# Performance work log

Hardware: AMD Instinct MI355X
Metric: run time of the kernel (lower is better)

## Reference

```python
import jax, jax.numpy as jnp
import numpy as np

SCALE = 0.5          # centroids_input_scale
MAX_STRIDE = 16      # centroids_max_stride
CM_STRIDE = 2        # centroids_confmaps_stride (backbone overall stride)
THRESH = 0.2         # peak_threshold
CROP = 160           # crop_size
K = 32               # max peaks per sample (ragged -> dense+mask)
PATCH = 5            # integral-refinement patch size (sleap default)


def setup_inputs() -> dict:
    key = jax.random.key(0)
    k1, k2, k3 = jax.random.split(key, 3)
    full_imgs = jax.random.uniform(k1, (16, 1024, 1024, 1), jnp.float32)
    w1 = jax.random.normal(k2, (5, 5, 1, 32), jnp.float32) * 0.1
    b1 = jnp.zeros((32,), jnp.float32)
    w2 = jax.random.normal(k3, (5, 5, 32, 1), jnp.float32) * 0.1
    b2 = jnp.zeros((1,), jnp.float32)
    return {"full_imgs": full_imgs, "w1": w1, "b1": b1, "w2": w2, "b2": b2}


def _conv(x, w, stride):
    return jax.lax.conv_general_dilated(
        x, w, (stride, stride), 'SAME',
        dimension_numbers=('NHWC', 'HWIO', 'NHWC'))


def _centroid_model(x, w1, b1, w2, b2):
    h = jax.nn.relu(_conv(x, w1, CM_STRIDE) + b1)
    return jax.nn.sigmoid(_conv(h, w2, 1) + b2)  # [B,Hc,Wc,1]


def _forward(full_imgs, w1, b1, w2, b2):
    B, H, W, C = full_imgs.shape
    # --- resize_image + pad_to_stride ---
    hs, ws = int(H * SCALE), int(W * SCALE)
    imgs = jax.image.resize(full_imgs, (B, hs, ws, C), 'bilinear')
    ph, pw = (-hs) % MAX_STRIDE, (-ws) % MAX_STRIDE
    imgs = jnp.pad(imgs, ((0, 0), (0, ph), (0, pw), (0, 0)))
    # --- centroid confmaps ---
    cms = _centroid_model(imgs, w1, b1, w2, b2)[..., 0]  # [B,Hc,Wc]
    Hc, Wc = cms.shape[1], cms.shape[2]
    # --- find_local_peaks: 3x3 NMS + threshold, top-K per sample ---
    mx = jax.lax.reduce_window(cms, -jnp.inf, jax.lax.max,
                               (1, 3, 3), (1, 1, 1), 'SAME')
    is_peak = (cms >= mx) & (cms > THRESH)
    scores = jnp.where(is_peak, cms, -jnp.inf).reshape(B, -1)
    vals, idx = jax.lax.top_k(scores, K)            # [B,K]
    valid = jnp.isfinite(vals)                      # [B,K] bool
    py = idx // Wc
    px = idx % Wc
    # --- integral refinement over PATCH x PATCH (zero outside bounds) ---
    off = jnp.arange(PATCH) - (PATCH - 1) // 2      # [-2..2]
    yy = py[..., None, None] + off[None, None, :, None]   # [B,K,P,P]
    xx = px[..., None, None] + off[None, None, None, :]
    inb = (yy >= 0) & (yy < Hc) & (xx >= 0) & (xx < Wc)
    yc = jnp.clip(yy, 0, Hc - 1)
    xc = jnp.clip(xx, 0, Wc - 1)
    bidx = jnp.arange(B)[:, None, None, None]
    patches = cms[bidx, yc, xc] * inb               # [B,K,P,P]
    gv = patches.sum((-2, -1)) + 1e-12
    fo = off.astype(cms.dtype)
    dx = (patches * fo[None, None, None, :]).sum((-2, -1)) / gv
    dy = (patches * fo[None, None, :, None]).sum((-2, -1)) / gv
    # --- map back to full-image coords ---
    cx = (px.astype(cms.dtype) + dx) * CM_STRIDE / SCALE
    cy = (py.astype(cms.dtype) + dy) * CM_STRIDE / SCALE
    cx = jnp.where(valid, cx, CROP / 2)
    cy = jnp.where(valid, cy, CROP / 2)
    centroid_vals = jnp.where(valid, vals, 0.0)
    crop_offsets = jnp.stack([cx - CROP / 2, cy - CROP / 2], axis=-1)  # (x,y)
    # --- crop_bboxes: bilinear crop of CROPxCROP, (CROP-1)-pixel span ---
    gi = jnp.arange(CROP, dtype=cms.dtype)
    sy = (cy - (CROP - 1) / 2)[..., None] + gi      # [B,K,CROP] row coords
    sx = (cx - (CROP - 1) / 2)[..., None] + gi      # [B,K,CROP] col coords
    y0 = jnp.floor(sy); x0 = jnp.floor(sx)
    wy = (sy - y0)[..., :, None, None]              # [B,K,CROP,1,1]
    wx = (sx - x0)[..., None, :, None]              # [B,K,1,CROP,1]
    yi0 = jnp.clip(y0.astype(jnp.int32), 0, H - 1)
    yi1 = jnp.clip(y0.astype(jnp.int32) + 1, 0, H - 1)
    xi0 = jnp.clip(x0.astype(jnp.int32), 0, W - 1)
    xi1 = jnp.clip(x0.astype(jnp.int32) + 1, 0, W - 1)

    def gath(yi, xi):  # -> [B,K,CROP,CROP,C]
        return full_imgs[bidx, yi[..., :, None], xi[..., None, :], :]

    top = gath(yi0, xi0) * (1 - wx) + gath(yi0, xi1) * wx
    bot = gath(yi1, xi0) * (1 - wx) + gath(yi1, xi1) * wx
    crops = top * (1 - wy) + bot * wy
    # crop_and_resize extrapolation_value=0 outside the image
    inr = (((sy >= 0) & (sy <= H - 1))[..., :, None]
           & ((sx >= 0) & (sx <= W - 1))[..., None, :])
    crops = crops * inr[..., None] * valid[..., None, None, None]
    return crops, crop_offsets, centroid_vals, valid


def reference(full_imgs, w1, b1, w2, b2):
    return _forward(full_imgs, w1, b1, w2, b2)
```

## Files before the change

kernel.cpp:

```cpp
#include <hip/hip_runtime.h>
#include <math.h>

#define BATCH 16
#define HF 1024
#define WF 1024
#define HS 512
#define WS2 512
#define HC 256
#define WC 256
#define KMAX 32
#define CAP 16384
#define CROPSZ 160
#define CNT_STRIDE 16
#define NCHUNK 16
#define CHUNK 1024

#define OFF_IMGS 0UL
#define OFF_CMS  16777216UL
#define OFF_KEYS 20971520UL
#define OFF_CNT  23068672UL
#define OFF_CX   23070720UL
#define OFF_CY   (OFF_CX + 2048UL)
#define OFF_VLD  (OFF_CY + 2048UL)
#define OFF_CAND (OFF_VLD + 2048UL)

#define OUT_CROPS 0
#define OUT_OFFS  13107200
#define OUT_VALS  13108224
#define OUT_VALID 13108736

__global__ __launch_bounds__(256) void resize_kernel(const float* __restrict__ full,
                                                     float* __restrict__ imgs,
                                                     int* __restrict__ counts) {
    if (blockIdx.x == 0 && blockIdx.y == 0 && threadIdx.x < BATCH * CNT_STRIDE)
        counts[threadIdx.x] = 0;
    __shared__ float simg[10][1024];
    int tid = threadIdx.x;
    int y0 = blockIdx.x << 2;
    int b = blockIdx.y;
    const float* base = full + ((size_t)b << 20);
#pragma unroll
    for (int s = 0; s < 10; ++s) {
        int r = 2 * y0 - 1 + s;
        r = r < 0 ? 0 : (r > HF - 1 ? HF - 1 : r);
        ((float4*)simg[s])[tid] = ((const float4*)(base + r * WF))[tid];
    }
    __syncthreads();
    const float w4[4] = {0.125f, 0.375f, 0.375f, 0.125f};
#pragma unroll
    for (int p = 0; p < 2; ++p) {
        int x = tid + 256 * p;
        float wx[4];
        int rx[4];
        float sx = 0.f;
#pragma unroll
        for (int ii = 0; ii < 4; ++ii) {
            int c = 2 * x - 1 + ii;
            float wc = (c >= 0 && c < WF) ? w4[ii] : 0.f;
            wx[ii] = wc; sx += wc;
            rx[ii] = c < 0 ? 0 : (c >= WF ? WF - 1 : c);
        }
#pragma unroll
        for (int r = 0; r < 4; ++r) {
            int yy = y0 + r;
            float sy = 0.f;
            float wy[4];
#pragma unroll
            for (int j = 0; j < 4; ++j) {
                int rr = 2 * yy - 1 + j;
                float w = (rr >= 0 && rr < HF) ? w4[j] : 0.f;
                wy[j] = w; sy += w;
            }
            float acc = 0.f;
#pragma unroll
            for (int j = 0; j < 4; ++j) {
                float rowacc = 0.f;
                const float* sr = simg[2 * r + j];
#pragma unroll
                for (int ii = 0; ii < 4; ++ii) rowacc += wx[ii] * sr[rx[ii]];
                acc += wy[j] * rowacc;
            }
            imgs[((size_t)b << 18) + (yy << 9) + x] = acc * (1.f / (sy * sx));
        }
    }
}

__global__ __launch_bounds__(256) void conv_fused2_kernel(
    const float* __restrict__ imgs, const float* __restrict__ w1,
    const float* __restrict__ b1, const float* __restrict__ w2,
    const float* __restrict__ b2, float* __restrict__ cms) {
    __shared__ float simg[75][76];
    __shared__ float4 sh[36][37];
    int tid = threadIdx.x;
    int b = blockIdx.y;
    int Y0 = (blockIdx.x >> 3) << 5;
    int X0 = (blockIdx.x & 7) << 5;

    const float* ib = imgs + ((size_t)b << 18);
    int r0 = 2 * Y0 - 5, c0 = 2 * X0 - 5;
    for (int i = tid; i < 75 * 76; i += 256) {
        int r = i / 76, c = i - r * 76;
        int gy = r0 + r, gx = c0 + c;
        float v = 0.f;
        if ((unsigned)gy < 512u && (unsigned)gx < 512u)
            v = ib[(gy << 9) + gx];
        simg[r][c] = v;
    }

    bool c1act = tid < 216;
    int ghy = tid / 6;
    int ghx0 = (tid - ghy * 6) * 6;
    const float* c1base = &simg[2 * ghy][2 * ghx0];
    float4* shw = &sh[ghy][ghx0];
    bool rowok = (unsigned)(Y0 - 2 + ghy) < 256u;
    int gx0 = X0 - 2 + ghx0;

    int cx = tid & 31;
    int ry0 = (tid >> 5) << 2;
    const float4* hb = &sh[ry0][cx];
    float4 zv0 = make_float4(0.f, 0.f, 0.f, 0.f);
    float4 zv1 = zv0, zv2 = zv0, zv3 = zv0;

    for (int q = 0; q < 8; ++q) {
        float4 wq[25];
        const float4* w14 = (const float4*)w1;
#pragma unroll
        for (int t = 0; t < 25; ++t) wq[t] = w14[t * 8 + q];
        float4 bq = ((const float4*)b1)[q];

        __syncthreads();

        if (c1act) {
            float4 acc[6];
#pragma unroll
            for (int j = 0; j < 6; ++j) acc[j] = bq;
#pragma unroll
            for (int ky = 0; ky < 5; ++ky) {
                const float* rp = c1base + ky * 76;
                float4 f0 = *(const float4*)(rp);
                float4 f1 = *(const float4*)(rp + 4);
                float4 f2 = *(const float4*)(rp + 8);
                float4 f3 = *(const float4*)(rp + 12);
                float f[16] = {f0.x, f0.y, f0.z, f0.w, f1.x, f1.y, f1.z, f1.w,
                               f2.x, f2.y, f2.z, f2.w, f3.x, f3.y, f3.z, f3.w};
#pragma unroll
                for (int j = 0; j < 6; ++j)
#pragma unroll
                    for (int kx = 0; kx < 5; ++kx) {
                        float v = f[2 * j + kx];
                        float4 w = wq[ky * 5 + kx];
                        acc[j].x += v * w.x; acc[j].y += v * w.y;
                        acc[j].z += v * w.z; acc[j].w += v * w.w;
                    }
            }
#pragma unroll
            for (int j = 0; j < 6; ++j) {
                float4 r;
                bool ok = rowok && ((unsigned)(gx0 + j) < 256u);
                r.x = ok ? fmaxf(acc[j].x, 0.f) : 0.f;
                r.y = ok ? fmaxf(acc[j].y, 0.f) : 0.f;
                r.z = ok ? fmaxf(acc[j].z, 0.f) : 0.f;
                r.w = ok ? fmaxf(acc[j].w, 0.f) : 0.f;
                shw[j] = r;
            }
        }

        const float4* w24 = (const float4*)w2;
#pragma unroll
        for (int t = 0; t < 25; ++t) wq[t] = w24[t * 8 + q];

        __syncthreads();

#pragma unroll
        for (int rr = 0; rr < 8; ++rr) {
#pragma unroll
            for (int kx = 0; kx < 5; ++kx) {
                float4 hv = hb[rr * 37 + kx];
#pragma unroll
                for (int j = 0; j < 4; ++j) {
                    int ky = rr - j;
                    if (ky < 0 || ky > 4) continue;
                    float4 w = wq[ky * 5 + kx];
                    if (j == 0) {
                        zv0.x += hv.x * w.x; zv0.y += hv.y * w.y;
                        zv0.z += hv.z * w.z; zv0.w += hv.w * w.w;
                    } else if (j == 1) {
                        zv1.x += hv.x * w.x; zv1.y += hv.y * w.y;
                        zv1.z += hv.z * w.z; zv1.w += hv.w * w.w;
                    } else if (j == 2) {
                        zv2.x += hv.x * w.x; zv2.y += hv.y * w.y;
                        zv2.z += hv.z * w.z; zv2.w += hv.w * w.w;
                    } else {
                        zv3.x += hv.x * w.x; zv3.y += hv.y * w.y;
                        zv3.z += hv.z * w.z; zv3.w += hv.w * w.w;
                    }
                }
            }
        }
    }

    float bb = b2[0];
    float z0 = bb + zv0.x + zv0.y + zv0.z + zv0.w;
    float z1 = bb + zv1.x + zv1.y + zv1.z + zv1.w;
    float z2 = bb + zv2.x + zv2.y + zv2.z + zv2.w;
    float z3 = bb + zv3.x + zv3.y + zv3.z + zv3.w;
    size_t ob = ((size_t)b << 16) + ((size_t)(Y0 + ry0) << 8) + (X0 + cx);
    cms[ob]       = 1.f / (1.f + expf(-z0));
    cms[ob + 256] = 1.f / (1.f + expf(-z1));
    cms[ob + 512] = 1.f / (1.f + expf(-z2));
    cms[ob + 768] = 1.f / (1.f + expf(-z3));
}

__global__ __launch_bounds__(256) void peak_scan_kernel(
    const float* __restrict__ cms, unsigned long long* __restrict__ keys,
    int* __restrict__ counts) {
    int b = blockIdx.x >> 8;
    int y = blockIdx.x & 255;
    int x = threadIdx.x;
    const float* cb = cms + ((size_t)b << 16);
    __shared__ float rows[3][256];
    __shared__ int lcnt, lbase;
    if (x == 0) lcnt = 0;
#pragma unroll
    for (int j = 0; j < 3; ++j) {
        int yy = y - 1 + j;
        rows[j][x] = (yy >= 0 && yy < HC) ? cb[yy * WC + x] : -INFINITY;
    }
    __syncthreads();
    float c = rows[1][x];
    bool peak = (c > 0.2f);
    if (peak) {
#pragma unroll
        for (int j = 0; j < 3; ++j) {
            float r0 = rows[j][x];
            float rl = (x > 0)   ? rows[j][x - 1] : -INFINITY;
            float rr = (x < 255) ? rows[j][x + 1] : -INFINITY;
            if (fmaxf(r0, fmaxf(rl, rr)) > c) peak = false;
        }
    }
    int p = -1;
    if (peak) p = atomicAdd(&lcnt, 1);
    __syncthreads();
    if (x == 0) lbase = lcnt ? atomicAdd(&counts[b * CNT_STRIDE], lcnt) : 0;
    __syncthreads();
    if (peak) {
        int pos = lbase + p;
        if (pos < CAP) {
            int i = y * WC + x;
            unsigned long long key =
                ((unsigned long long)__float_as_uint(c) << 32) |
                (unsigned long long)(0xFFFFFFFFu - (unsigned)i);
            keys[(size_t)b * CAP + pos] = key;
        }
    }
}

__global__ __launch_bounds__(64) void topk_stage_a(
    const unsigned long long* __restrict__ keys, const int* __restrict__ counts,
    unsigned long long* __restrict__ cand) {
    int b = blockIdx.x >> 4;
    int chunk = blockIdx.x & 15;
    int lane = threadIdx.x;
    int cnt = counts[b * CNT_STRIDE]; if (cnt > CAP) cnt = CAP;
    const unsigned long long* kb = keys + (size_t)b * CAP + chunk * CHUNK;
    int lim = cnt - chunk * CHUNK;
    unsigned long long v[16];
#pragma unroll
    for (int j = 0; j < 16; ++j) {
        int i = lane + (j << 6);
        v[j] = (i < lim) ? kb[i] : 0ULL;
    }
    unsigned long long* out = cand + (size_t)(b * NCHUNK + chunk) * KMAX;
    int k = 0;
    for (; k < KMAX; ++k) {
        unsigned long long best = v[0];
#pragma unroll
        for (int j = 1; j < 16; ++j) best = v[j] > best ? v[j] : best;
#pragma unroll
        for (int s = 1; s < 64; s <<= 1) {
            unsigned long long o = __shfl_xor(best, s, 64);
            if (o > best) best = o;
        }
        if (best == 0ULL) break;
        if (lane == 0) out[k] = best;
#pragma unroll
        for (int j = 0; j < 16; ++j) if (v[j] == best) v[j] = 0ULL;
    }
    if (lane >= k && lane < KMAX) out[lane] = 0ULL;
}

__global__ __launch_bounds__(64) void topk_stage_b(
    const float* __restrict__ cms, const unsigned long long* __restrict__ cand,
    float* __restrict__ out_off, float* __restrict__ out_vals,
    float* __restrict__ out_valid, float* __restrict__ ws_cx,
    float* __restrict__ ws_cy, float* __restrict__ ws_v) {
    int b = blockIdx.x;
    int lane = threadIdx.x;
    unsigned long long v[8];
#pragma unroll
    for (int j = 0; j < 8; ++j)
        v[j] = cand[(size_t)b * 512 + lane + (j << 6)];
    unsigned long long mysel = 0ULL;
    for (int k = 0; k < KMAX; ++k) {
        unsigned long long best = v[0];
#pragma unroll
        for (int j = 1; j < 8; ++j) best = v[j] > best ? v[j] : best;
#pragma unroll
        for (int s = 1; s < 64; s <<= 1) {
            unsigned long long o = __shfl_xor(best, s, 64);
            if (o > best) best = o;
        }
        if (best == 0ULL) break;
        if (lane == k) mysel = best;
#pragma unroll
        for (int j = 0; j < 8; ++j) if (v[j] == best) v[j] = 0ULL;
    }
    if (lane < KMAX) {
        unsigned long long key = mysel;
        bool valid = key != 0ULL;
        float cx = 80.f, cy = 80.f, val = 0.f;
        if (valid) {
            val = __uint_as_float((unsigned)(key >> 32));
            int idx = (int)(0xFFFFFFFFu - (unsigned)(key & 0xFFFFFFFFULL));
            int py = idx >> 8, px = idx & 255;
            const float* cb = cms + ((size_t)b << 16);
            float gv = 1e-12f, sdx = 0.f, sdy = 0.f;
#pragma unroll
            for (int oy = -2; oy <= 2; ++oy)
#pragma unroll
                for (int ox = -2; ox <= 2; ++ox) {
                    int yy = py + oy, xx = px + ox;
                    if (yy < 0 || yy >= HC || xx < 0 || xx >= WC) continue;
                    float pv = cb[yy * WC + xx];
                    gv += pv; sdx += pv * (float)ox; sdy += pv * (float)oy;
                }
            float dx = sdx / gv, dy = sdy / gv;
            cx = ((float)px + dx) * 4.f;
            cy = ((float)py + dy) * 4.f;
        }
        int o = b * KMAX + lane;
        out_off[o * 2 + 0] = cx - 80.f;
        out_off[o * 2 + 1] = cy - 80.f;
        out_vals[o] = val;
        out_valid[o] = valid ? 1.f : 0.f;
        ws_cx[o] = cx; ws_cy[o] = cy; ws_v[o] = valid ? 1.f : 0.f;
    }
}

__global__ __launch_bounds__(256) void crop_kernel(
    const float* __restrict__ full, const float* __restrict__ ws_cx,
    const float* __restrict__ ws_cy, const float* __restrict__ ws_v,
    float* __restrict__ out_crops) {
    int bidx = blockIdx.x;
    int cid = bidx / 100;
    int pp = (bidx - cid * 100) * 256 + threadIdx.x;
    int b = cid >> 5;
    float cx = ws_cx[cid], cy = ws_cy[cid], v = ws_v[cid];
    int row = pp / CROPSZ, col = pp - row * CROPSZ;
    float sy = cy - 79.5f + (float)row;
    float sx = cx - 79.5f + (float)col;
    float y0f = floorf(sy), x0f = floorf(sx);
    float wy = sy - y0f, wx = sx - x0f;
    int y0 = (int)y0f, x0 = (int)x0f;
    int yi0 = min(max(y0, 0), HF - 1);
    int yi1 = min(max(y0 + 1, 0), HF - 1);
    int xi0 = min(max(x0, 0), WF - 1);
    int xi1 = min(max(x0 + 1, 0), WF - 1);
    const float* base = full + ((size_t)b << 20);
    float t00 = base[yi0 * WF + xi0];
    float t01 = base[yi0 * WF + xi1];
    float t10 = base[yi1 * WF + xi0];
    float t11 = base[yi1 * WF + xi1];
    float top = t00 * (1.f - wx) + t01 * wx;
    float bot = t10 * (1.f - wx) + t11 * wx;
    float val = top * (1.f - wy) + bot * wy;
    float inr = (sy >= 0.f && sy <= (float)(HF - 1) &&
                 sx >= 0.f && sx <= (float)(WF - 1)) ? 1.f : 0.f;
    out_crops[(size_t)cid * (CROPSZ * CROPSZ) + pp] = val * inr * v;
}

extern "C" void kernel_launch(void* const* d_in, const int* in_sizes, int n_in,
                              void* d_out, int out_size, void* d_ws, size_t ws_size,
                              hipStream_t stream) {
    const float* full = (const float*)d_in[0];
    const float* w1   = (const float*)d_in[1];
    const float* b1   = (const float*)d_in[2];
    const float* w2   = (const float*)d_in[3];
    const float* b2   = (const float*)d_in[4];

    char* ws = (char*)d_ws;
    float* imgs = (float*)(ws + OFF_IMGS);
    float* cms  = (float*)(ws + OFF_CMS);
    unsigned long long* keys = (unsigned long long*)(ws + OFF_KEYS);
    int* counts = (int*)(ws + OFF_CNT);
    float* ws_cx = (float*)(ws + OFF_CX);
    float* ws_cy = (float*)(ws + OFF_CY);
    float* ws_v  = (float*)(ws + OFF_VLD);
    unsigned long long* cand = (unsigned long long*)(ws + OFF_CAND);

    float* out = (float*)d_out;
    float* out_crops = out + OUT_CROPS;
    float* out_off   = out + OUT_OFFS;
    float* out_vals  = out + OUT_VALS;
    float* out_valid = out + OUT_VALID;

    hipLaunchKernelGGL(resize_kernel, dim3(128, 16), dim3(256), 0, stream,
                       full, imgs, counts);

    hipLaunchKernelGGL(conv_fused2_kernel, dim3(64, 16), dim3(256), 0, stream,
                       imgs, w1, b1, w2, b2, cms);

    hipLaunchKernelGGL(peak_scan_kernel, dim3(4096), dim3(256), 0, stream,
                       cms, keys, counts);
    hipLaunchKernelGGL(topk_stage_a, dim3(256), dim3(64), 0, stream,
                       keys, counts, cand);
    hipLaunchKernelGGL(topk_stage_b, dim3(16), dim3(64), 0, stream,
                       cms, cand, out_off, out_vals, out_valid,
                       ws_cx, ws_cy, ws_v);
    hipLaunchKernelGGL(crop_kernel, dim3(51200), dim3(256), 0, stream,
                       full, ws_cx, ws_cy, ws_v, out_crops);
}
```

Baseline: 283.2 us.

## Pad resized image in global memory, read conv directly, batch crop rows

```diff
diff --git a/kernel.cpp b/kernel.cpp
--- a/kernel.cpp
+++ b/kernel.cpp
@@ -15,11 +15,15 @@
 #define NCHUNK 16
 #define CHUNK 1024
 
+#define IMGP_W 524
+#define IMGP_H 524
+#define IMGP_STRIDE (IMGP_W * IMGP_H)
+
 #define OFF_IMGS 0UL
-#define OFF_CMS  16777216UL
-#define OFF_KEYS 20971520UL
-#define OFF_CNT  23068672UL
-#define OFF_CX   23070720UL
+#define OFF_CMS  17572864UL
+#define OFF_KEYS (OFF_CMS + 4194304UL)
+#define OFF_CNT  (OFF_KEYS + 2097152UL)
+#define OFF_CX   (OFF_CNT + 2048UL)
 #define OFF_CY   (OFF_CX + 2048UL)
 #define OFF_VLD  (OFF_CY + 2048UL)
 #define OFF_CAND (OFF_VLD + 2048UL)
@@ -39,6 +43,17 @@
     int y0 = blockIdx.x << 2;
     int b = blockIdx.y;
     const float* base = full + ((size_t)b << 20);
+    float* ob = imgs + (size_t)b * IMGP_STRIDE;
+    if (tid < 48) {
+        int r = tid / 12, c = tid - (tid / 12) * 12;
+        int col = c < 5 ? c : 512 + c;
+        ob[(size_t)(5 + y0 + r) * IMGP_W + col] = 0.f;
+    }
+    if (blockIdx.x == 0)
+        for (int i = tid; i < 5 * IMGP_W; i += 256) ob[i] = 0.f;
+    if (blockIdx.x == 127)
+        for (int i = tid; i < 7 * IMGP_W; i += 256)
+            ob[(size_t)517 * IMGP_W + i] = 0.f;
 #pragma unroll
     for (int s = 0; s < 10; ++s) {
         int r = 2 * y0 - 1 + s;
@@ -80,37 +95,27 @@
                 for (int ii = 0; ii < 4; ++ii) rowacc += wx[ii] * sr[rx[ii]];
                 acc += wy[j] * rowacc;
             }
-            imgs[((size_t)b << 18) + (yy << 9) + x] = acc * (1.f / (sy * sx));
-        }
-    }
-}
-
-__global__ __launch_bounds__(256) void conv_fused2_kernel(
+            ob[(size_t)(5 + yy) * IMGP_W + 5 + x] = acc * (1.f / (sy * sx));
+        }
+    }
+}
+
+__global__ __launch_bounds__(256, 4) void conv_fused2_kernel(
     const float* __restrict__ imgs, const float* __restrict__ w1,
     const float* __restrict__ b1, const float* __restrict__ w2,
     const float* __restrict__ b2, float* __restrict__ cms) {
-    __shared__ float simg[75][76];
     __shared__ float4 sh[36][37];
     int tid = threadIdx.x;
     int b = blockIdx.y;
     int Y0 = (blockIdx.x >> 3) << 5;
     int X0 = (blockIdx.x & 7) << 5;
-
-    const float* ib = imgs + ((size_t)b << 18);
-    int r0 = 2 * Y0 - 5, c0 = 2 * X0 - 5;
-    for (int i = tid; i < 75 * 76; i += 256) {
-        int r = i / 76, c = i - r * 76;
-        int gy = r0 + r, gx = c0 + c;
-        float v = 0.f;
-        if ((unsigned)gy < 512u && (unsigned)gx < 512u)
-            v = ib[(gy << 9) + gx];
-        simg[r][c] = v;
-    }
+    const float* ib = imgs + (size_t)b * IMGP_STRIDE;
 
     bool c1act = tid < 216;
     int ghy = tid / 6;
     int ghx0 = (tid - ghy * 6) * 6;
-    const float* c1base = &simg[2 * ghy][2 * ghx0];
+    const float* gbase = ib + (size_t)(2 * Y0 + 2 * ghy) * IMGP_W
+                            + (2 * X0 + 2 * ghx0);
     float4* shw = &sh[ghy][ghx0];
     bool rowok = (unsigned)(Y0 - 2 + ghy) < 256u;
     int gx0 = X0 - 2 + ghx0;
@@ -128,6 +133,10 @@
         for (int t = 0; t < 25; ++t) wq[t] = w14[t * 8 + q];
         float4 bq = ((const float4*)b1)[q];
 
+        int qoff = 0;
+        asm volatile("" : "+v"(qoff));
+        const float* gb = gbase + qoff;
+
         __syncthreads();
 
         if (c1act) {
@@ -136,7 +145,7 @@
             for (int j = 0; j < 6; ++j) acc[j] = bq;
 #pragma unroll
             for (int ky = 0; ky < 5; ++ky) {
-                const float* rp = c1base + ky * 76;
+                const float* rp = gb + ky * IMGP_W;
                 float4 f0 = *(const float4*)(rp);
                 float4 f1 = *(const float4*)(rp + 4);
                 float4 f2 = *(const float4*)(rp + 8);
@@ -352,31 +361,41 @@
     const float* __restrict__ ws_cy, const float* __restrict__ ws_v,
     float* __restrict__ out_crops) {
     int bidx = blockIdx.x;
-    int cid = bidx / 100;
-    int pp = (bidx - cid * 100) * 256 + threadIdx.x;
+    int cid = bidx / 25;
+    int p = (bidx - cid * 25) * 256 + threadIdx.x;
     int b = cid >> 5;
     float cx = ws_cx[cid], cy = ws_cy[cid], v = ws_v[cid];
-    int row = pp / CROPSZ, col = pp - row * CROPSZ;
-    float sy = cy - 79.5f + (float)row;
+    int rg = p / CROPSZ;
+    int col = p - rg * CROPSZ;
+    int r0 = rg << 2;
     float sx = cx - 79.5f + (float)col;
-    float y0f = floorf(sy), x0f = floorf(sx);
-    float wy = sy - y0f, wx = sx - x0f;
-    int y0 = (int)y0f, x0 = (int)x0f;
-    int yi0 = min(max(y0, 0), HF - 1);
-    int yi1 = min(max(y0 + 1, 0), HF - 1);
+    float x0f = floorf(sx);
+    float wx = sx - x0f;
+    int x0 = (int)x0f;
     int xi0 = min(max(x0, 0), WF - 1);
     int xi1 = min(max(x0 + 1, 0), WF - 1);
+    float syb = cy - 79.5f + (float)r0;
+    float y0f = floorf(syb);
+    float wy = syb - y0f;
+    int y0 = (int)y0f;
     const float* base = full + ((size_t)b << 20);
-    float t00 = base[yi0 * WF + xi0];
-    float t01 = base[yi0 * WF + xi1];
-    float t10 = base[yi1 * WF + xi0];
-    float t11 = base[yi1 * WF + xi1];
-    float top = t00 * (1.f - wx) + t01 * wx;
-    float bot = t10 * (1.f - wx) + t11 * wx;
-    float val = top * (1.f - wy) + bot * wy;
-    float inr = (sy >= 0.f && sy <= (float)(HF - 1) &&
-                 sx >= 0.f && sx <= (float)(WF - 1)) ? 1.f : 0.f;
-    out_crops[(size_t)cid * (CROPSZ * CROPSZ) + pp] = val * inr * v;
+    float rv[5];
+#pragma unroll
+    for (int i = 0; i < 5; ++i) {
+        int yy = min(max(y0 + i, 0), HF - 1);
+        float a = base[yy * WF + xi0];
+        float c = base[yy * WF + xi1];
+        rv[i] = a * (1.f - wx) + c * wx;
+    }
+    bool xin = (sx >= 0.f && sx <= (float)(WF - 1));
+    size_t ob = (size_t)cid * (CROPSZ * CROPSZ) + r0 * CROPSZ + col;
+#pragma unroll
+    for (int i = 0; i < 4; ++i) {
+        float sy = syb + (float)i;
+        float val = rv[i] * (1.f - wy) + rv[i + 1] * wy;
+        float inr = (xin && sy >= 0.f && sy <= (float)(HF - 1)) ? 1.f : 0.f;
+        out_crops[ob + i * CROPSZ] = val * inr * v;
+    }
 }
 
 extern "C" void kernel_launch(void* const* d_in, const int* in_sizes, int n_in,
@@ -417,6 +436,6 @@
     hipLaunchKernelGGL(topk_stage_b, dim3(16), dim3(64), 0, stream,
                        cms, cand, out_off, out_vals, out_valid,
                        ws_cx, ws_cy, ws_v);
-    hipLaunchKernelGGL(crop_kernel, dim3(51200), dim3(256), 0, stream,
+    hipLaunchKernelGGL(crop_kernel, dim3(12800), dim3(256), 0, stream,
                        full, ws_cx, ws_cy, ws_v, out_crops);
 }
```

Measured after the change: 262.7 us. -7.2%, faster.
